# Kernel optimization log

Hardware: AMD Instinct MI355X
Metric: run time of the kernel (lower is better)

The kernel has to match this reference:

```python
import jax, jax.numpy as jnp
import numpy as np

NUM_GRAPHS = 16  # static number of graphs for pooling
BN_EPS = 1e-5


def gat_layer(x, W, a_src, a_dst, src, dst, N, concat):
    # x: (N, Fin), W: (H, Fin, Fout), a_src/a_dst: (H, Fout)
    Wh = jnp.einsum('ni,hio->hno', x, W)                      # (H, N, Fout)
    e_src = jnp.einsum('hno,ho->hn', Wh, a_src)               # (H, N)
    e_dst = jnp.einsum('hno,ho->hn', Wh, a_dst)               # (H, N)
    e = jax.nn.leaky_relu(e_src[:, src] + e_dst[:, dst], 0.2)  # (H, E)
    # edge softmax over incoming edges per dst; torch code starts max at 0
    seg_max = jax.vmap(lambda eh: jax.ops.segment_max(eh, dst, num_segments=N))(e)
    e_max = jnp.maximum(seg_max, 0.0)                         # (H, N)
    exp_e = jnp.exp(e - e_max[:, dst])                        # (H, E)
    exp_sum = jax.vmap(lambda eh: jax.ops.segment_sum(eh, dst, num_segments=N))(exp_e)
    attn = exp_e / (exp_sum[:, dst] + 1e-8)                   # (H, E)
    msgs = attn[:, :, None] * Wh[:, src]                      # (H, E, Fout)
    out = jax.vmap(lambda m: jax.ops.segment_sum(m, dst, num_segments=N))(msgs)  # (H, N, Fout)
    if concat:
        out = jnp.transpose(out, (1, 0, 2)).reshape(N, -1)
    else:
        out = out.mean(axis=0)
    return out, attn


def batchnorm(h, gamma, beta):
    mu = h.mean(axis=0)
    var = h.var(axis=0)
    return (h - mu) / jnp.sqrt(var + BN_EPS) * gamma + beta


def setup_inputs() -> dict:
    key = jax.random.key(0)
    ks = jax.random.split(key, 20)
    N, E = 50000, 400000
    IN, HID, H, NC = 262, 128, 4, 2

    def xavier(k, shape):
        fan_in, fan_out = shape[-2], shape[-1]
        lim = np.sqrt(6.0 / (fan_in + fan_out))
        return jax.random.uniform(k, shape, jnp.float32, -lim, lim)

    x = jax.random.normal(ks[0], (N, IN), jnp.float32)
    edge_index = jax.random.randint(ks[1], (2, E), 0, N, jnp.int64)
    batch = jnp.sort(jax.random.randint(ks[2], (N,), 0, NUM_GRAPHS, jnp.int64))

    return {
        'x': x, 'edge_index': edge_index, 'batch': batch,
        'W1': xavier(ks[3], (H, IN, HID)),
        'a_src1': xavier(ks[4], (H, HID, 1)).squeeze(-1),
        'a_dst1': xavier(ks[5], (H, HID, 1)).squeeze(-1),
        'W2': xavier(ks[6], (1, HID * H, HID)),
        'a_src2': xavier(ks[7], (1, HID, 1)).squeeze(-1),
        'a_dst2': xavier(ks[8], (1, HID, 1)).squeeze(-1),
        'bn1_g': jnp.ones((HID * H,), jnp.float32),
        'bn1_b': jnp.zeros((HID * H,), jnp.float32),
        'bn2_g': jnp.ones((HID,), jnp.float32),
        'bn2_b': jnp.zeros((HID,), jnp.float32),
        'cls_w1': xavier(ks[9], (HID, HID // 2)),
        'cls_b1': jnp.zeros((HID // 2,), jnp.float32),
        'cls_w2': xavier(ks[10], (HID // 2, NC)),
        'cls_b2': jnp.zeros((NC,), jnp.float32),
        'ep_w1': xavier(ks[11], (HID * 2, HID)),
        'ep_b1': jnp.zeros((HID,), jnp.float32),
        'ep_w2': xavier(ks[12], (HID, 1)),
        'ep_b2': jnp.zeros((1,), jnp.float32),
    }


def reference(x, edge_index, batch, W1, a_src1, a_dst1, W2, a_src2, a_dst2,
              bn1_g, bn1_b, bn2_g, bn2_b, cls_w1, cls_b1, cls_w2, cls_b2,
              ep_w1, ep_b1, ep_w2, ep_b2):
    N = x.shape[0]
    src, dst = edge_index[0], edge_index[1]

    h1, _ = gat_layer(x, W1, a_src1, a_dst1, src, dst, N, concat=True)
    h1 = batchnorm(jax.nn.elu(h1), bn1_g, bn1_b)

    h2, attn2 = gat_layer(h1, W2, a_src2, a_dst2, src, dst, N, concat=False)
    h2 = batchnorm(jax.nn.elu(h2), bn2_g, bn2_b)

    # global mean pool over graphs
    sums = jax.ops.segment_sum(h2, batch, num_segments=NUM_GRAPHS)
    counts = jax.ops.segment_sum(jnp.ones((N,), h2.dtype), batch, num_segments=NUM_GRAPHS)
    graph_repr = sums / jnp.clip(counts, 1.0)[:, None]

    logits = jax.nn.relu(graph_repr @ cls_w1 + cls_b1) @ cls_w2 + cls_b2

    edge_feat = jnp.concatenate([h2[src], h2[dst]], axis=1)  # (E, 2*hidden)
    importance = jax.nn.sigmoid(
        (jax.nn.relu(edge_feat @ ep_w1 + ep_b1) @ ep_w2 + ep_b2).squeeze(-1))

    gat_attention = jnp.transpose(attn2, (1, 0))  # (E, 1)
    return logits, h2, importance, gat_attention
```

## Files before the change

### kernel.cpp

```cpp
#include <hip/hip_runtime.h>
#include <hip/hip_bf16.h>
#include <math.h>

typedef __hip_bfloat16 bf16;
typedef __bf16 bf16x8 __attribute__((ext_vector_type(8)));
typedef __bf16 bf16x2v __attribute__((ext_vector_type(2)));
typedef float f32x4 __attribute__((ext_vector_type(4)));

#define NN 50000
#define EE 400000
#define FIN 262
#define KP1 288
#define HID 128
#define NH 4
#define C1 512
#define NGR 16
#define SCAN_NB ((NN + 255) / 256)

__device__ __forceinline__ float b2f(bf16 x){ return __bfloat162float(x); }
__device__ __forceinline__ bf16 f2b(float x){ return __float2bfloat16(x); }
__device__ __forceinline__ float lrelu(float v){ return v >= 0.f ? v : 0.2f * v; }
__device__ __forceinline__ float eluf(float v){ return v > 0.f ? v : expm1f(v); }

__global__ void zero_words(unsigned int* __restrict__ p, int n) {
  int i = blockIdx.x * 256 + threadIdx.x;
  if (i < n) p[i] = 0u;
}

__global__ __launch_bounds__(256)
void gemm_mfma(const bf16* __restrict__ A, const bf16* __restrict__ Bt,
               bf16* __restrict__ C, int M, int K, int Ncols,
               const float* __restrict__ sc, const float* __restrict__ sh) {
  __shared__ __align__(16) __bf16 As[2][128 * 40];
  __shared__ __align__(16) __bf16 Bs[2][128 * 40];
  int bm = blockIdx.y * 128, bn = blockIdx.x * 128;
  int tid = threadIdx.x;
  int wave = tid >> 6, lane = tid & 63;
  int quad = lane >> 4, l16 = lane & 15;
  int wm = (wave >> 1) * 64, wn = (wave & 1) * 64;
  int rowA = (tid * 8) >> 5;
  int colT = (tid * 8) & 31;
  int gm0 = bm + rowA, gm1 = bm + rowA + 64;
  int gn0 = bn + rowA, gn1 = bn + rowA + 64;
  const uint4 zz = {0u, 0u, 0u, 0u};

  f32x4 acc[4][4];
  #pragma unroll
  for (int i = 0; i < 4; ++i)
    #pragma unroll
    for (int j = 0; j < 4; ++j)
      acc[i][j] = (f32x4){0.f, 0.f, 0.f, 0.f};

  uint4 a0, a1, b0, b1;

  auto xf = [&](uint4 v, int kb) -> uint4 {
    if (sc == nullptr) return v;
    bf16x8 a8 = *(bf16x8*)&v;
    float4 c0 = *(const float4*)(sc + kb);
    float4 c1 = *(const float4*)(sc + kb + 4);
    float4 h0 = *(const float4*)(sh + kb);
    float4 h1 = *(const float4*)(sh + kb + 4);
    bf16x8 t8;
    t8[0] = (__bf16)((float)a8[0] * c0.x + h0.x);
    t8[1] = (__bf16)((float)a8[1] * c0.y + h0.y);
    t8[2] = (__bf16)((float)a8[2] * c0.z + h0.z);
    t8[3] = (__bf16)((float)a8[3] * c0.w + h0.w);
    t8[4] = (__bf16)((float)a8[4] * c1.x + h1.x);
    t8[5] = (__bf16)((float)a8[5] * c1.y + h1.y);
    t8[6] = (__bf16)((float)a8[6] * c1.z + h1.z);
    t8[7] = (__bf16)((float)a8[7] * c1.w + h1.w);
    return *(uint4*)&t8;
  };
  auto ld = [&](int k0) {
    a0 = (gm0 < M) ? *(const uint4*)(A + (size_t)gm0 * K + k0 + colT) : zz;
    a1 = (gm1 < M) ? *(const uint4*)(A + (size_t)gm1 * K + k0 + colT) : zz;
    b0 = (gn0 < Ncols) ? *(const uint4*)(Bt + (size_t)gn0 * K + k0 + colT) : zz;
    b1 = (gn1 < Ncols) ? *(const uint4*)(Bt + (size_t)gn1 * K + k0 + colT) : zz;
  };
  auto st = [&](int buf, int k0) {
    *(uint4*)(&As[buf][rowA * 40 + colT])        = xf(a0, k0 + colT);
    *(uint4*)(&As[buf][(rowA + 64) * 40 + colT]) = xf(a1, k0 + colT);
    *(uint4*)(&Bs[buf][rowA * 40 + colT])        = b0;
    *(uint4*)(&Bs[buf][(rowA + 64) * 40 + colT]) = b1;
  };

  int nt = K >> 5;
  ld(0);
  st(0, 0);
  __syncthreads();

  for (int t = 0; t < nt; ++t) {
    int cur = t & 1;
    bool more = (t + 1 < nt);
    if (more) ld((t + 1) << 5);

    bf16x8 af[4], bfr[4];
    #pragma unroll
    for (int i = 0; i < 4; ++i)
      af[i] = *(const bf16x8*)(&As[cur][(wm + i * 16 + l16) * 40 + quad * 8]);
    #pragma unroll
    for (int j = 0; j < 4; ++j)
      bfr[j] = *(const bf16x8*)(&Bs[cur][(wn + j * 16 + l16) * 40 + quad * 8]);
    #pragma unroll
    for (int i = 0; i < 4; ++i)
      #pragma unroll
      for (int j = 0; j < 4; ++j)
        acc[i][j] = __builtin_amdgcn_mfma_f32_16x16x32_bf16(af[i], bfr[j], acc[i][j], 0, 0, 0);

    if (more) st(cur ^ 1, (t + 1) << 5);
    __syncthreads();
  }

  #pragma unroll
  for (int i = 0; i < 4; ++i) {
    #pragma unroll
    for (int r = 0; r < 4; ++r) {
      int gm = bm + wm + i * 16 + quad * 4 + r;
      if (gm >= M) continue;
      #pragma unroll
      for (int j = 0; j < 4; ++j) {
        int gn = bn + wn + j * 16 + l16;
        C[(size_t)gm * Ncols + gn] = f2b(acc[i][j][r]);
      }
    }
  }
}

__global__ void conv_x(const float* __restrict__ x, bf16* __restrict__ xb) {
  int i = blockIdx.x * 256 + threadIdx.x;
  if (i >= NN * KP1) return;
  int row = i / KP1, col = i - row * KP1;
  xb[i] = (col < FIN) ? f2b(x[(size_t)row * FIN + col]) : f2b(0.f);
}
__global__ void prep_b1t(const float* __restrict__ W1, bf16* __restrict__ B1t) {
  int i = blockIdx.x * 256 + threadIdx.x;
  if (i >= C1 * KP1) return;
  int n = i / KP1, k = i - n * KP1;
  int h = n >> 7, o = n & 127;
  B1t[i] = (k < FIN) ? f2b(W1[((size_t)h * FIN + k) * HID + o]) : f2b(0.f);
}
__global__ void prep_b2t(const float* __restrict__ W2, bf16* __restrict__ B2t) {
  int i = blockIdx.x * 256 + threadIdx.x;
  if (i >= HID * C1) return;
  int n = i >> 9, k = i & 511;
  B2t[i] = f2b(W2[(size_t)k * HID + n]);
}
__global__ void prep_bpt(const float* __restrict__ epw1, bf16* __restrict__ BPt) {
  int i = blockIdx.x * 256 + threadIdx.x;
  if (i >= 256 * HID) return;
  int n = i >> 7, k = i & 127;
  float v = (n < 128) ? epw1[(size_t)k * HID + n] : epw1[(size_t)(128 + k) * HID + (n - 128)];
  BPt[i] = f2b(v);
}

__global__ void edot_all(const bf16* __restrict__ Wh1, const float* __restrict__ av,
                         const float* __restrict__ bv, float* __restrict__ es1,
                         float* __restrict__ ed1) {
  int wid = threadIdx.x >> 6, lane = threadIdx.x & 63;
  int n = blockIdx.x * 4 + wid;
  if (n >= NN) return;
  int h = lane >> 4, c16 = lane & 15;
  int fbase = h * HID + c16 * 8;
  bf16x8 r = *(const bf16x8*)(Wh1 + (size_t)n * C1 + fbase);
  float s1 = 0.f, s2 = 0.f;
  #pragma unroll
  for (int j = 0; j < 8; ++j) {
    float rv = (float)r[j];
    s1 += rv * av[fbase + j];
    s2 += rv * bv[fbase + j];
  }
  #pragma unroll
  for (int off = 8; off > 0; off >>= 1) {
    s1 += __shfl_xor(s1, off);
    s2 += __shfl_xor(s2, off);
  }
  if (c16 == 0) { es1[n * 4 + h] = s1; ed1[n * 4 + h] = s2; }
}

__global__ void edot1(const bf16* __restrict__ Wh, const float* __restrict__ av,
                      const float* __restrict__ bv, float* __restrict__ es,
                      float* __restrict__ ed) {
  int wid = threadIdx.x >> 6, lane = threadIdx.x & 63;
  int r = blockIdx.x * 4 + wid;
  if (r >= NN) return;
  const bf16* row = Wh + (size_t)r * HID;
  float w0 = b2f(row[lane]), w1 = b2f(row[lane + 64]);
  float s1 = w0 * av[lane] + w1 * av[lane + 64];
  float s2 = w0 * bv[lane] + w1 * bv[lane + 64];
  #pragma unroll
  for (int off = 32; off > 0; off >>= 1) {
    s1 += __shfl_xor(s1, off);
    s2 += __shfl_xor(s2, off);
  }
  if (lane == 0) { es[r] = s1; ed[r] = s2; }
}

__global__ void count_kernel(const int* __restrict__ dst, int* __restrict__ deg, int E) {
  int e = blockIdx.x * blockDim.x + threadIdx.x;
  if (e >= E) return;
  int d = dst[e];
  if ((unsigned)d < NN) atomicAdd(&deg[d], 1);
}

__global__ void scan_p1(const int* __restrict__ deg, int* __restrict__ bsum) {
  __shared__ int s[256];
  int t = threadIdx.x;
  int i = blockIdx.x * 256 + t;
  s[t] = (i < NN) ? deg[i] : 0;
  __syncthreads();
  #pragma unroll
  for (int off = 128; off > 0; off >>= 1) {
    if (t < off) s[t] += s[t + off];
    __syncthreads();
  }
  if (t == 0) bsum[blockIdx.x] = s[0];
}
__global__ void scan_p2(const int* __restrict__ bsum, int* __restrict__ boff,
                        int* __restrict__ total_out) {
  __shared__ int s[256];
  int t = threadIdx.x;
  s[t] = (t < SCAN_NB) ? bsum[t] : 0;
  __syncthreads();
  if (t == 0) {
    int r = 0;
    for (int i = 0; i < SCAN_NB; ++i) { int v = s[i]; s[i] = r; r += v; }
    total_out[0] = r;
  }
  __syncthreads();
  if (t < SCAN_NB) boff[t] = s[t];
}
__global__ void scan_p3(const int* __restrict__ deg, const int* __restrict__ boff,
                        int* __restrict__ rowptr, int* __restrict__ cursor) {
  __shared__ int s[256];
  int t = threadIdx.x;
  int i = blockIdx.x * 256 + t;
  int v = (i < NN) ? deg[i] : 0;
  s[t] = v;
  __syncthreads();
  #pragma unroll
  for (int off = 1; off < 256; off <<= 1) {
    int add = (t >= off) ? s[t - off] : 0;
    __syncthreads();
    s[t] += add;
    __syncthreads();
  }
  if (i < NN) {
    int pos = boff[blockIdx.x] + s[t] - v;
    rowptr[i] = pos;
    cursor[i] = pos;
  }
}

__global__ void scatter_kernel(const int* __restrict__ src, const int* __restrict__ dst,
                               int* __restrict__ cursor, int* __restrict__ csr_s,
                               int* __restrict__ csr_d, int* __restrict__ csr_e, int E) {
  int e = blockIdx.x * blockDim.x + threadIdx.x;
  if (e >= E) return;
  int d = dst[e];
  if ((unsigned)d >= NN) return;
  int s = src[e]; if ((unsigned)s >= NN) s = 0;
  int p = atomicAdd(&cursor[d], 1);
  if ((unsigned)p < (unsigned)E) { csr_s[p] = s; csr_d[p] = d; csr_e[p] = e; }
}

__global__ void logits1(const int* __restrict__ csr_s, const int* __restrict__ csr_d,
                        const float4* __restrict__ es1, const float4* __restrict__ ed1,
                        float4* __restrict__ v1, int* __restrict__ m1i) {
  int j = blockIdx.x * 256 + threadIdx.x;
  if (j >= EE) return;
  int s = csr_s[j]; if ((unsigned)s >= NN) s = 0;
  int d = csr_d[j]; if ((unsigned)d >= NN) d = 0;
  float4 a = es1[s], bb = ed1[d];
  float4 v;
  v.x = lrelu(a.x + bb.x);
  v.y = lrelu(a.y + bb.y);
  v.z = lrelu(a.z + bb.z);
  v.w = lrelu(a.w + bb.w);
  v1[j] = v;
  if (v.x > 0.f) atomicMax(&m1i[d * 4 + 0], __float_as_int(v.x));
  if (v.y > 0.f) atomicMax(&m1i[d * 4 + 1], __float_as_int(v.y));
  if (v.z > 0.f) atomicMax(&m1i[d * 4 + 2], __float_as_int(v.z));
  if (v.w > 0.f) atomicMax(&m1i[d * 4 + 3], __float_as_int(v.w));
}

__global__ void logits2(const int* __restrict__ csr_s, const int* __restrict__ csr_d,
                        const float* __restrict__ es2, const float* __restrict__ ed2,
                        float* __restrict__ v2, int* __restrict__ m2i) {
  int j = blockIdx.x * 256 + threadIdx.x;
  if (j >= EE) return;
  int s = csr_s[j]; if ((unsigned)s >= NN) s = 0;
  int d = csr_d[j]; if ((unsigned)d >= NN) d = 0;
  float v = lrelu(es2[s] + ed2[d]);
  v2[j] = v;
  if (v > 0.f) atomicMax(&m2i[d], __float_as_int(v));
}

__global__ __launch_bounds__(256, 6)
void agg1_all(const int* __restrict__ csr_s, const int* __restrict__ rowptr,
              const float* __restrict__ lg, const float* __restrict__ mx,
              const bf16* __restrict__ Wh1, bf16* __restrict__ h1) {
  int wid = threadIdx.x >> 6, lane = threadIdx.x & 63;
  int node = blockIdx.x * 4 + wid;
  if (node >= NN) return;
  int b = rowptr[node], e = rowptr[node + 1];
  if (b < 0) b = 0; if (e > EE) e = EE;
  int h = lane >> 4;
  float m = mx[node * 4 + h];
  float sum = 0.f;
  float acc[8] = {};
  const bf16* W = Wh1 + lane * 8;
  int j = b;
  for (; j + 8 <= e; j += 8) {
    int s_[8]; float w[8];
    #pragma unroll
    for (int i = 0; i < 8; ++i) { s_[i] = csr_s[j + i]; w[i] = lg[(j + i) * 4 + h]; }
    bf16x8 r[8];
    #pragma unroll
    for (int i = 0; i < 8; ++i)
      r[i] = *(const bf16x8*)(W + (size_t)s_[i] * C1);
    #pragma unroll
    for (int i = 0; i < 8; ++i) {
      float p = __expf(w[i] - m);
      sum += p;
      #pragma unroll
      for (int k = 0; k < 8; ++k) acc[k] += p * (float)r[i][k];
    }
  }
  if (j + 4 <= e) {
    int s_[4]; float w[4];
    #pragma unroll
    for (int i = 0; i < 4; ++i) { s_[i] = csr_s[j + i]; w[i] = lg[(j + i) * 4 + h]; }
    bf16x8 r[4];
    #pragma unroll
    for (int i = 0; i < 4; ++i)
      r[i] = *(const bf16x8*)(W + (size_t)s_[i] * C1);
    #pragma unroll
    for (int i = 0; i < 4; ++i) {
      float p = __expf(w[i] - m);
      sum += p;
      #pragma unroll
      for (int k = 0; k < 8; ++k) acc[k] += p * (float)r[i][k];
    }
    j += 4;
  }
  for (; j < e; ++j) {
    int s0 = csr_s[j];
    float p = __expf(lg[j * 4 + h] - m);
    bf16x8 r0 = *(const bf16x8*)(W + (size_t)s0 * C1);
    sum += p;
    #pragma unroll
    for (int k = 0; k < 8; ++k) acc[k] += p * (float)r0[k];
  }
  float scale = 1.f / (sum + 1e-8f);
  bf16x8 o;
  #pragma unroll
  for (int k = 0; k < 8; ++k) o[k] = (__bf16)eluf(acc[k] * scale);
  *(bf16x8*)(h1 + (size_t)node * C1 + lane * 8) = o;
}

__global__ __launch_bounds__(256, 8)
void agg2_all(const int* __restrict__ csr_s, const int* __restrict__ rowptr,
              const float* __restrict__ lg, const float* __restrict__ mx,
              const bf16* __restrict__ Wh2, bf16* __restrict__ h2p,
              float* __restrict__ invs2) {
  int tid = threadIdx.x;
  int l16 = tid & 15;
  int node = blockIdx.x * 16 + (tid >> 4);
  if (node >= NN) return;
  int b = rowptr[node], e = rowptr[node + 1];
  if (b < 0) b = 0; if (e > EE) e = EE;
  float m = mx[node];
  float sum = 0.f;
  float acc[8] = {};
  const bf16* W = Wh2 + l16 * 8;
  int j = b;
  for (; j + 4 <= e; j += 4) {
    int s_[4]; float w[4];
    #pragma unroll
    for (int i = 0; i < 4; ++i) { s_[i] = csr_s[j + i]; w[i] = lg[j + i]; }
    bf16x8 r[4];
    #pragma unroll
    for (int i = 0; i < 4; ++i)
      r[i] = *(const bf16x8*)(W + (size_t)s_[i] * HID);
    #pragma unroll
    for (int i = 0; i < 4; ++i) {
      float p = __expf(w[i] - m);
      sum += p;
      #pragma unroll
      for (int k = 0; k < 8; ++k) acc[k] += p * (float)r[i][k];
    }
  }
  for (; j < e; ++j) {
    int s0 = csr_s[j];
    float p = __expf(lg[j] - m);
    bf16x8 r0 = *(const bf16x8*)(W + (size_t)s0 * HID);
    sum += p;
    #pragma unroll
    for (int k = 0; k < 8; ++k) acc[k] += p * (float)r0[k];
  }
  float scale = 1.f / (sum + 1e-8f);
  bf16x8 o;
  #pragma unroll
  for (int k = 0; k < 8; ++k) o[k] = (__bf16)eluf(acc[k] * scale);
  *(bf16x8*)(h2p + (size_t)node * HID + l16 * 8) = o;
  if (l16 == 0) invs2[node] = scale;
}

__global__ void attn_csr(const int* __restrict__ csr_d, const int* __restrict__ csr_e,
                         const float* __restrict__ lg, const float* __restrict__ mx,
                         const float* __restrict__ invs2, float* __restrict__ out) {
  int j = blockIdx.x * 256 + threadIdx.x;
  if (j >= EE) return;
  int d = csr_d[j]; if ((unsigned)d >= NN) d = 0;
  int e = csr_e[j]; if ((unsigned)e >= EE) return;
  out[e] = __expf(lg[j] - mx[d]) * invs2[d];
}

__global__ void stats_ro(const bf16* __restrict__ X, float* __restrict__ cs,
                         float* __restrict__ cq, int Nrows, int C) {
  int c = threadIdx.x;
  int rpb = (Nrows + gridDim.x - 1) / gridDim.x;
  int r0 = blockIdx.x * rpb, r1 = min(r0 + rpb, Nrows);
  float s = 0.f, s2 = 0.f;
  for (int r = r0; r < r1; ++r) {
    float v = b2f(X[(size_t)r * C + c]);
    s += v; s2 += v * v;
  }
  atomicAdd(&cs[c], s);
  atomicAdd(&cq[c], s2);
}

__global__ void bn_coef(const float* __restrict__ cs, const float* __restrict__ cq,
                        const float* __restrict__ gamma, const float* __restrict__ beta,
                        float* __restrict__ sc, float* __restrict__ sh, int C, float invN) {
  int c = blockIdx.x * 256 + threadIdx.x;
  if (c >= C) return;
  float mu = cs[c] * invN;
  float var = cq[c] * invN - mu * mu;
  float g = rsqrtf(fmaxf(var, 0.f) + 1e-5f) * gamma[c];
  sc[c] = g;
  sh[c] = beta[c] - mu * g;
}

__global__ void bn_out(const bf16* __restrict__ in, float* __restrict__ out2,
                       const float* __restrict__ sc, const float* __restrict__ sh) {
  int i = blockIdx.x * 256 + threadIdx.x;
  if (i >= NN * HID / 8) return;
  int c8 = (i & 15) * 8;
  bf16x8 v = *(const bf16x8*)(in + (size_t)i * 8);
  float o[8];
  #pragma unroll
  for (int k = 0; k < 8; ++k) o[k] = (float)v[k] * sc[c8 + k] + sh[c8 + k];
  *(float4*)(out2 + (size_t)i * 8)     = make_float4(o[0], o[1], o[2], o[3]);
  *(float4*)(out2 + (size_t)i * 8 + 4) = make_float4(o[4], o[5], o[6], o[7]);
}

__global__ __launch_bounds__(256)
void pool_kernel(const bf16* __restrict__ h2, const int* __restrict__ batch,
                 float* __restrict__ pooled) {
  int t = threadIdx.x;
  int f = t & 127, half = t >> 7;
  int r0 = blockIdx.x * 32;
  int g_cur = -1;
  float acc = 0.f;
  #pragma unroll
  for (int i = 0; i < 16; ++i) {
    int r = r0 + half + 2 * i;
    if (r >= NN) break;
    int g = batch[r]; if ((unsigned)g >= NGR) g = 0;
    float v = b2f(h2[(size_t)r * HID + f]);
    if (g != g_cur) {
      if (g_cur >= 0) atomicAdd(&pooled[g_cur * HID + f], acc);
      g_cur = g; acc = 0.f;
    }
    acc += v;
  }
  if (g_cur >= 0) atomicAdd(&pooled[g_cur * HID + f], acc);
}

__global__ void cnt_kernel(const int* __restrict__ batch, float* __restrict__ cnt) {
  int g = threadIdx.x;
  if (g >= NGR) return;
  int a = 0, b = NN;
  while (a < b) { int m = (a + b) >> 1; if (batch[m] < g) a = m + 1; else b = m; }
  int lb = a;
  a = 0; b = NN;
  while (a < b) { int m = (a + b) >> 1; if (batch[m] <= g) a = m + 1; else b = m; }
  cnt[g] = (float)(a - lb);
}

__global__ void cls_kernel(const float* __restrict__ pooled, const float* __restrict__ cnt,
                           const float* __restrict__ sc2, const float* __restrict__ sh2,
                           const float* __restrict__ w1, const float* __restrict__ b1,
                           const float* __restrict__ w2, const float* __restrict__ b2,
                           float* __restrict__ out) {
  __shared__ float repr[NGR * HID];
  __shared__ float hid[NGR * 64];
  int t = threadIdx.x;
  for (int i = t; i < NGR * HID; i += 128) {
    int g = i >> 7, c = i & 127;
    float c_ = cnt[g];
    repr[i] = (c_ > 0.f) ? (pooled[i] / c_ * sc2[c] + sh2[c]) : 0.f;
  }
  __syncthreads();
  for (int i = t; i < NGR * 64; i += 128) {
    int g = i >> 6, j = i & 63;
    float s = b1[j];
    for (int c = 0; c < HID; ++c) s += repr[g * HID + c] * w1[c * 64 + j];
    hid[i] = fmaxf(s, 0.f);
  }
  __syncthreads();
  if (t < NGR * 2) {
    int g = t >> 1, k = t & 1;
    float s = b2[k];
    for (int j = 0; j < 64; ++j) s += hid[g * 64 + j] * w2[j * 2 + k];
    out[t] = s;
  }
}

__global__ __launch_bounds__(256)
void eimp_kernel(const int* __restrict__ csr_s, const int* __restrict__ csr_d,
                 const int* __restrict__ csr_e, const bf16* __restrict__ PQ,
                 const float* __restrict__ b1, const float* __restrict__ w2,
                 const float* __restrict__ b2, float* __restrict__ out) {
  int tid = threadIdx.x;
  int wave = tid >> 6, lane = tid & 63;
  int g = lane >> 4, l16 = lane & 15;
  int slot = blockIdx.x * 16 + wave * 4 + g;
  if (slot >= EE) return;
  int s = csr_s[slot]; if ((unsigned)s >= NN) s = 0;
  int d = csr_d[slot]; if ((unsigned)d >= NN) d = 0;
  int e = csr_e[slot]; if ((unsigned)e >= EE) return;
  bf16x8 p = *(const bf16x8*)(PQ + (size_t)s * 256 + l16 * 8);
  bf16x8 q = *(const bf16x8*)(PQ + (size_t)d * 256 + 128 + l16 * 8);
  float acc = 0.f;
  #pragma unroll
  for (int r = 0; r < 8; ++r) {
    int jj = l16 * 8 + r;
    float hh = (float)p[r] + (float)q[r] + b1[jj];
    hh = fmaxf(hh, 0.f);
    acc += hh * w2[jj];
  }
  #pragma unroll
  for (int off = 8; off > 0; off >>= 1) acc += __shfl_xor(acc, off);
  if (l16 == 0) {
    float z = acc + b2[0];
    out[e] = 1.f / (1.f + expf(-z));
  }
}

extern "C" void kernel_launch(void* const* d_in, const int* in_sizes, int n_in,
                              void* d_out, int out_size, void* d_ws, size_t ws_size,
                              hipStream_t stream) {
  const float* x      = (const float*)d_in[0];
  const int*   ei     = (const int*)d_in[1];
  const int*   batch  = (const int*)d_in[2];
  const float* W1     = (const float*)d_in[3];
  const float* a_src1 = (const float*)d_in[4];
  const float* a_dst1 = (const float*)d_in[5];
  const float* W2     = (const float*)d_in[6];
  const float* a_src2 = (const float*)d_in[7];
  const float* a_dst2 = (const float*)d_in[8];
  const float* bn1_g  = (const float*)d_in[9];
  const float* bn1_b  = (const float*)d_in[10];
  const float* bn2_g  = (const float*)d_in[11];
  const float* bn2_b  = (const float*)d_in[12];
  const float* cls_w1 = (const float*)d_in[13];
  const float* cls_b1 = (const float*)d_in[14];
  const float* cls_w2 = (const float*)d_in[15];
  const float* cls_b2 = (const float*)d_in[16];
  const float* ep_w1  = (const float*)d_in[17];
  const float* ep_b1  = (const float*)d_in[18];
  const float* ep_w2  = (const float*)d_in[19];
  const float* ep_b2  = (const float*)d_in[20];

  const int* srcp = ei;
  const int* dstp = ei + EE;

  char* base = (char*)d_ws;
  bf16* xb   = (bf16*)(base);
  bf16* h1   = (bf16*)(base);
  bf16* Wh1  = (bf16*)(base + 51200000);
  bf16* Wh2  = (bf16*)(base + 51200000);
  bf16* PQ   = (bf16*)(base + 51200000);
  bf16* h2p  = (bf16*)(base + 76800000);
  float* es1   = (float*)(base + 102400000);
  float* ed1   = (float*)(base + 103200000);
  float* v2csr = (float*)(base + 102400000);
  int*   m1i   = (int*)(base + 104000000);
  int*   m2i   = (int*)(base + 104800000);
  int*   deg   = (int*)(base + 105000000);
  float* stats = (float*)(base + 105200000);
  float* cs1 = stats,        *cq1 = stats + 512;
  float* cs2 = stats + 1024, *cq2 = stats + 1152;
  float* pooled = stats + 1280;
  float* cnt    = stats + 3328;
  float* sc1   = (float*)(base + 105213376);
  float* sh1   = (float*)(base + 105215424);
  float* sc2   = (float*)(base + 105217472);
  float* sh2   = (float*)(base + 105217984);
  float* es2   = (float*)(base + 105218496);
  float* ed2   = (float*)(base + 105418496);
  float* invs2 = (float*)(base + 105618496);
  int*   cursor= (int*)(base + 105818496);
  int*   rowptr= (int*)(base + 106018496);
  int*   bsum  = (int*)(base + 106218560);
  int*   boff  = bsum + 256;
  int*   csr_s = (int*)(base + 106220608);
  int*   csr_d = (int*)(base + 107820608);
  int*   csr_e = (int*)(base + 109420608);
  float* v1csr = (float*)(base + 111020608);
  bf16*  B1t   = (bf16*)(base + 117420608);
  bf16*  B2t   = (bf16*)(base + 117715520);
  bf16*  BPt   = (bf16*)(base + 117846592);

  float* out        = (float*)d_out;
  float* out_logits = out;
  float* out_h2     = out + 32;
  float* out_imp    = out + 32 + (size_t)NN * HID;
  float* out_attn   = out_imp + EE;

  zero_words<<<(303344 + 255) / 256, 256, 0, stream>>>((unsigned int*)m1i, 303344);

  conv_x<<<(NN * KP1 + 255) / 256, 256, 0, stream>>>(x, xb);
  prep_b1t<<<(C1 * KP1 + 255) / 256, 256, 0, stream>>>(W1, B1t);
  prep_b2t<<<(HID * C1 + 255) / 256, 256, 0, stream>>>(W2, B2t);
  prep_bpt<<<(256 * HID + 255) / 256, 256, 0, stream>>>(ep_w1, BPt);

  count_kernel<<<(EE + 255) / 256, 256, 0, stream>>>(dstp, deg, EE);
  scan_p1<<<SCAN_NB, 256, 0, stream>>>(deg, bsum);
  scan_p2<<<1, 256, 0, stream>>>(bsum, boff, rowptr + NN);
  scan_p3<<<SCAN_NB, 256, 0, stream>>>(deg, boff, rowptr, cursor);
  scatter_kernel<<<(EE + 255) / 256, 256, 0, stream>>>(srcp, dstp, cursor,
                                                       csr_s, csr_d, csr_e, EE);

  dim3 g1(C1 / 128, (NN + 127) / 128);
  gemm_mfma<<<g1, 256, 0, stream>>>(xb, B1t, Wh1, NN, KP1, C1, nullptr, nullptr);
  edot_all<<<(NN + 3) / 4, 256, 0, stream>>>(Wh1, a_src1, a_dst1, es1, ed1);
  logits1<<<(EE + 255) / 256, 256, 0, stream>>>(csr_s, csr_d, (const float4*)es1,
                                                (const float4*)ed1, (float4*)v1csr, m1i);
  agg1_all<<<(NN + 3) / 4, 256, 0, stream>>>(csr_s, rowptr, v1csr,
                                             (const float*)m1i, Wh1, h1);

  stats_ro<<<400, C1, 0, stream>>>(h1, cs1, cq1, NN, C1);
  bn_coef<<<2, 256, 0, stream>>>(cs1, cq1, bn1_g, bn1_b, sc1, sh1, C1, 1.f / NN);

  dim3 g2(1, (NN + 127) / 128);
  gemm_mfma<<<g2, 256, 0, stream>>>(h1, B2t, Wh2, NN, C1, HID, sc1, sh1);
  edot1<<<(NN + 3) / 4, 256, 0, stream>>>(Wh2, a_src2, a_dst2, es2, ed2);
  logits2<<<(EE + 255) / 256, 256, 0, stream>>>(csr_s, csr_d, es2, ed2, v2csr, m2i);
  agg2_all<<<(NN + 15) / 16, 256, 0, stream>>>(csr_s, rowptr, v2csr,
                                               (const float*)m2i, Wh2, h2p, invs2);
  attn_csr<<<(EE + 255) / 256, 256, 0, stream>>>(csr_d, csr_e, v2csr,
                                                 (const float*)m2i, invs2, out_attn);

  pool_kernel<<<(NN + 31) / 32, 256, 0, stream>>>(h2p, batch, pooled);
  cnt_kernel<<<1, 64, 0, stream>>>(batch, cnt);

  stats_ro<<<400, HID, 0, stream>>>(h2p, cs2, cq2, NN, HID);
  bn_coef<<<1, 256, 0, stream>>>(cs2, cq2, bn2_g, bn2_b, sc2, sh2, HID, 1.f / NN);
  bn_out<<<(NN * HID / 8 + 255) / 256, 256, 0, stream>>>(h2p, out_h2, sc2, sh2);

  cls_kernel<<<1, 128, 0, stream>>>(pooled, cnt, sc2, sh2,
                                    cls_w1, cls_b1, cls_w2, cls_b2, out_logits);

  dim3 gpq(2, (NN + 127) / 128);
  gemm_mfma<<<gpq, 256, 0, stream>>>(h2p, BPt, PQ, NN, HID, 256, sc2, sh2);
  eimp_kernel<<<(EE + 15) / 16, 256, 0, stream>>>(csr_s, csr_d, csr_e, PQ,
                                                  ep_b1, ep_w2, ep_b2, out_imp);
}
```

Measured before the change: 654.3 us.

## Fuse fp32 conversion and attention dots into GEMM, merge pool with BN output

The first GEMM now reads fp32 x directly and converts it to bf16 while staging into shared memory, which removes the separate conv_x pass and its bf16 buffer. Both GAT GEMMs compute the per-node attention dot products (e_src, e_dst) in their epilogue, reducing across lanes and accumulating with atomics, so the edot kernels go away. The BN2 output write is folded into the pooling kernel, and the count kernel is merged into the classifier kernel. In exchange, the fp32 A loads use narrower float2 accesses with bounds checks, and the atomic accumulation requires zeroing a larger region.

Result: no change. 644.7 us (-1.5%).

```diff
diff --git a/kernel.cpp b/kernel.cpp
--- a/kernel.cpp
+++ b/kernel.cpp
@@ -28,9 +28,12 @@
 }
 
 __global__ __launch_bounds__(256)
-void gemm_mfma(const bf16* __restrict__ A, const bf16* __restrict__ Bt,
-               bf16* __restrict__ C, int M, int K, int Ncols,
-               const float* __restrict__ sc, const float* __restrict__ sh) {
+void gemm_mfma(const bf16* __restrict__ A, const float* __restrict__ Af32, int srcW,
+               const bf16* __restrict__ Bt, bf16* __restrict__ C,
+               int M, int K, int Ncols,
+               const float* __restrict__ sc, const float* __restrict__ sh,
+               const float* __restrict__ av, const float* __restrict__ bv,
+               float* __restrict__ esp, float* __restrict__ edp, int dstride) {
   __shared__ __align__(16) __bf16 As[2][128 * 40];
   __shared__ __align__(16) __bf16 Bs[2][128 * 40];
   int bm = blockIdx.y * 128, bn = blockIdx.x * 128;
@@ -52,6 +55,7 @@
       acc[i][j] = (f32x4){0.f, 0.f, 0.f, 0.f};
 
   uint4 a0, a1, b0, b1;
+  float fa0[8], fa1[8];
 
   auto xf = [&](uint4 v, int kb) -> uint4 {
     if (sc == nullptr) return v;
@@ -71,15 +75,38 @@
     t8[7] = (__bf16)((float)a8[7] * c1.w + h1.w);
     return *(uint4*)&t8;
   };
+  auto ldf = [&](float* F, int gm, int k0) {
+    #pragma unroll
+    for (int p = 0; p < 4; ++p) {
+      int col = k0 + colT + p * 2;
+      float2 v = make_float2(0.f, 0.f);
+      if (gm < M && col < srcW)
+        v = *(const float2*)(Af32 + (size_t)gm * srcW + col);
+      F[p * 2] = v.x; F[p * 2 + 1] = v.y;
+    }
+  };
   auto ld = [&](int k0) {
-    a0 = (gm0 < M) ? *(const uint4*)(A + (size_t)gm0 * K + k0 + colT) : zz;
-    a1 = (gm1 < M) ? *(const uint4*)(A + (size_t)gm1 * K + k0 + colT) : zz;
+    if (Af32) {
+      ldf(fa0, gm0, k0);
+      ldf(fa1, gm1, k0);
+    } else {
+      a0 = (gm0 < M) ? *(const uint4*)(A + (size_t)gm0 * K + k0 + colT) : zz;
+      a1 = (gm1 < M) ? *(const uint4*)(A + (size_t)gm1 * K + k0 + colT) : zz;
+    }
     b0 = (gn0 < Ncols) ? *(const uint4*)(Bt + (size_t)gn0 * K + k0 + colT) : zz;
     b1 = (gn1 < Ncols) ? *(const uint4*)(Bt + (size_t)gn1 * K + k0 + colT) : zz;
   };
   auto st = [&](int buf, int k0) {
-    *(uint4*)(&As[buf][rowA * 40 + colT])        = xf(a0, k0 + colT);
-    *(uint4*)(&As[buf][(rowA + 64) * 40 + colT]) = xf(a1, k0 + colT);
+    if (Af32) {
+      bf16x8 t0, t1;
+      #pragma unroll
+      for (int p = 0; p < 8; ++p) { t0[p] = (__bf16)fa0[p]; t1[p] = (__bf16)fa1[p]; }
+      *(uint4*)(&As[buf][rowA * 40 + colT])        = *(uint4*)&t0;
+      *(uint4*)(&As[buf][(rowA + 64) * 40 + colT]) = *(uint4*)&t1;
+    } else {
+      *(uint4*)(&As[buf][rowA * 40 + colT])        = xf(a0, k0 + colT);
+      *(uint4*)(&As[buf][(rowA + 64) * 40 + colT]) = xf(a1, k0 + colT);
+    }
     *(uint4*)(&Bs[buf][rowA * 40 + colT])        = b0;
     *(uint4*)(&Bs[buf][(rowA + 64) * 40 + colT]) = b1;
   };
@@ -124,14 +151,39 @@
       }
     }
   }
-}
-
-__global__ void conv_x(const float* __restrict__ x, bf16* __restrict__ xb) {
-  int i = blockIdx.x * 256 + threadIdx.x;
-  if (i >= NN * KP1) return;
-  int row = i / KP1, col = i - row * KP1;
-  xb[i] = (col < FIN) ? f2b(x[(size_t)row * FIN + col]) : f2b(0.f);
-}
+
+  if (esp) {
+    float avj[4], bvj[4];
+    #pragma unroll
+    for (int j = 0; j < 4; ++j) {
+      int gn = bn + wn + j * 16 + l16;
+      avj[j] = av[gn]; bvj[j] = bv[gn];
+    }
+    int hoff = (dstride == 4) ? (bn >> 7) : 0;
+    #pragma unroll
+    for (int i = 0; i < 4; ++i)
+      #pragma unroll
+      for (int r = 0; r < 4; ++r) {
+        float pa = 0.f, pb = 0.f;
+        #pragma unroll
+        for (int j = 0; j < 4; ++j) {
+          float v = acc[i][j][r];
+          pa += v * avj[j]; pb += v * bvj[j];
+        }
+        #pragma unroll
+        for (int off = 8; off > 0; off >>= 1) {
+          pa += __shfl_xor(pa, off);
+          pb += __shfl_xor(pb, off);
+        }
+        int gm = bm + wm + i * 16 + quad * 4 + r;
+        if (l16 == 0 && gm < M) {
+          atomicAdd(&esp[gm * dstride + hoff], pa);
+          atomicAdd(&edp[gm * dstride + hoff], pb);
+        }
+      }
+  }
+}
+
 __global__ void prep_b1t(const float* __restrict__ W1, bf16* __restrict__ B1t) {
   int i = blockIdx.x * 256 + threadIdx.x;
   if (i >= C1 * KP1) return;
@@ -151,48 +203,6 @@
   int n = i >> 7, k = i & 127;
   float v = (n < 128) ? epw1[(size_t)k * HID + n] : epw1[(size_t)(128 + k) * HID + (n - 128)];
   BPt[i] = f2b(v);
-}
-
-__global__ void edot_all(const bf16* __restrict__ Wh1, const float* __restrict__ av,
-                         const float* __restrict__ bv, float* __restrict__ es1,
-                         float* __restrict__ ed1) {
-  int wid = threadIdx.x >> 6, lane = threadIdx.x & 63;
-  int n = blockIdx.x * 4 + wid;
-  if (n >= NN) return;
-  int h = lane >> 4, c16 = lane & 15;
-  int fbase = h * HID + c16 * 8;
-  bf16x8 r = *(const bf16x8*)(Wh1 + (size_t)n * C1 + fbase);
-  float s1 = 0.f, s2 = 0.f;
-  #pragma unroll
-  for (int j = 0; j < 8; ++j) {
-    float rv = (float)r[j];
-    s1 += rv * av[fbase + j];
-    s2 += rv * bv[fbase + j];
-  }
-  #pragma unroll
-  for (int off = 8; off > 0; off >>= 1) {
-    s1 += __shfl_xor(s1, off);
-    s2 += __shfl_xor(s2, off);
-  }
-  if (c16 == 0) { es1[n * 4 + h] = s1; ed1[n * 4 + h] = s2; }
-}
-
-__global__ void edot1(const bf16* __restrict__ Wh, const float* __restrict__ av,
-                      const float* __restrict__ bv, float* __restrict__ es,
-                      float* __restrict__ ed) {
-  int wid = threadIdx.x >> 6, lane = threadIdx.x & 63;
-  int r = blockIdx.x * 4 + wid;
-  if (r >= NN) return;
-  const bf16* row = Wh + (size_t)r * HID;
-  float w0 = b2f(row[lane]), w1 = b2f(row[lane + 64]);
-  float s1 = w0 * av[lane] + w1 * av[lane + 64];
-  float s2 = w0 * bv[lane] + w1 * bv[lane + 64];
-  #pragma unroll
-  for (int off = 32; off > 0; off >>= 1) {
-    s1 += __shfl_xor(s1, off);
-    s2 += __shfl_xor(s2, off);
-  }
-  if (lane == 0) { es[r] = s1; ed[r] = s2; }
 }
 
 __global__ void count_kernel(const int* __restrict__ dst, int* __restrict__ deg, int E) {
@@ -442,24 +452,13 @@
   sh[c] = beta[c] - mu * g;
 }
 
-__global__ void bn_out(const bf16* __restrict__ in, float* __restrict__ out2,
-                       const float* __restrict__ sc, const float* __restrict__ sh) {
-  int i = blockIdx.x * 256 + threadIdx.x;
-  if (i >= NN * HID / 8) return;
-  int c8 = (i & 15) * 8;
-  bf16x8 v = *(const bf16x8*)(in + (size_t)i * 8);
-  float o[8];
-  #pragma unroll
-  for (int k = 0; k < 8; ++k) o[k] = (float)v[k] * sc[c8 + k] + sh[c8 + k];
-  *(float4*)(out2 + (size_t)i * 8)     = make_float4(o[0], o[1], o[2], o[3]);
-  *(float4*)(out2 + (size_t)i * 8 + 4) = make_float4(o[4], o[5], o[6], o[7]);
-}
-
 __global__ __launch_bounds__(256)
-void pool_kernel(const bf16* __restrict__ h2, const int* __restrict__ batch,
-                 float* __restrict__ pooled) {
+void poolbn_kernel(const bf16* __restrict__ h2p, const int* __restrict__ batch,
+                   const float* __restrict__ sc, const float* __restrict__ sh,
+                   float* __restrict__ out_h2, float* __restrict__ pooled) {
   int t = threadIdx.x;
   int f = t & 127, half = t >> 7;
+  float scf = sc[f], shf = sh[f];
   int r0 = blockIdx.x * 32;
   int g_cur = -1;
   float acc = 0.f;
@@ -468,7 +467,8 @@
     int r = r0 + half + 2 * i;
     if (r >= NN) break;
     int g = batch[r]; if ((unsigned)g >= NGR) g = 0;
-    float v = b2f(h2[(size_t)r * HID + f]);
+    float v = b2f(h2p[(size_t)r * HID + f]) * scf + shf;
+    out_h2[(size_t)r * HID + f] = v;
     if (g != g_cur) {
       if (g_cur >= 0) atomicAdd(&pooled[g_cur * HID + f], acc);
       g_cur = g; acc = 0.f;
@@ -478,29 +478,27 @@
   if (g_cur >= 0) atomicAdd(&pooled[g_cur * HID + f], acc);
 }
 
-__global__ void cnt_kernel(const int* __restrict__ batch, float* __restrict__ cnt) {
-  int g = threadIdx.x;
-  if (g >= NGR) return;
-  int a = 0, b = NN;
-  while (a < b) { int m = (a + b) >> 1; if (batch[m] < g) a = m + 1; else b = m; }
-  int lb = a;
-  a = 0; b = NN;
-  while (a < b) { int m = (a + b) >> 1; if (batch[m] <= g) a = m + 1; else b = m; }
-  cnt[g] = (float)(a - lb);
-}
-
-__global__ void cls_kernel(const float* __restrict__ pooled, const float* __restrict__ cnt,
-                           const float* __restrict__ sc2, const float* __restrict__ sh2,
+__global__ void cls_kernel(const float* __restrict__ pooled, const int* __restrict__ batch,
                            const float* __restrict__ w1, const float* __restrict__ b1,
                            const float* __restrict__ w2, const float* __restrict__ b2,
                            float* __restrict__ out) {
   __shared__ float repr[NGR * HID];
   __shared__ float hid[NGR * 64];
+  __shared__ float scnt[NGR];
   int t = threadIdx.x;
+  if (t < NGR) {
+    int g = t;
+    int a = 0, b = NN;
+    while (a < b) { int m = (a + b) >> 1; if (batch[m] < g) a = m + 1; else b = m; }
+    int lb = a;
+    a = 0; b = NN;
+    while (a < b) { int m = (a + b) >> 1; if (batch[m] <= g) a = m + 1; else b = m; }
+    scnt[t] = (float)(a - lb);
+  }
+  __syncthreads();
   for (int i = t; i < NGR * HID; i += 128) {
-    int g = i >> 7, c = i & 127;
-    float c_ = cnt[g];
-    repr[i] = (c_ > 0.f) ? (pooled[i] / c_ * sc2[c] + sh2[c]) : 0.f;
+    int g = i >> 7;
+    repr[i] = pooled[i] / fmaxf(scnt[g], 1.f);
   }
   __syncthreads();
   for (int i = t; i < NGR * 64; i += 128) {
@@ -578,7 +576,6 @@
   const int* dstp = ei + EE;
 
   char* base = (char*)d_ws;
-  bf16* xb   = (bf16*)(base);
   bf16* h1   = (bf16*)(base);
   bf16* Wh1  = (bf16*)(base + 51200000);
   bf16* Wh2  = (bf16*)(base + 51200000);
@@ -587,20 +584,19 @@
   float* es1   = (float*)(base + 102400000);
   float* ed1   = (float*)(base + 103200000);
   float* v2csr = (float*)(base + 102400000);
-  int*   m1i   = (int*)(base + 104000000);
-  int*   m2i   = (int*)(base + 104800000);
-  int*   deg   = (int*)(base + 105000000);
-  float* stats = (float*)(base + 105200000);
+  float* es2   = (float*)(base + 104000000);
+  float* ed2   = (float*)(base + 104200000);
+  int*   m1i   = (int*)(base + 104400000);
+  int*   m2i   = (int*)(base + 105200000);
+  int*   deg   = (int*)(base + 105400000);
+  float* stats = (float*)(base + 105600000);
   float* cs1 = stats,        *cq1 = stats + 512;
   float* cs2 = stats + 1024, *cq2 = stats + 1152;
   float* pooled = stats + 1280;
-  float* cnt    = stats + 3328;
-  float* sc1   = (float*)(base + 105213376);
-  float* sh1   = (float*)(base + 105215424);
-  float* sc2   = (float*)(base + 105217472);
-  float* sh2   = (float*)(base + 105217984);
-  float* es2   = (float*)(base + 105218496);
-  float* ed2   = (float*)(base + 105418496);
+  float* sc1   = (float*)(base + 105613376);
+  float* sh1   = (float*)(base + 105615424);
+  float* sc2   = (float*)(base + 105617472);
+  float* sh2   = (float*)(base + 105617984);
   float* invs2 = (float*)(base + 105618496);
   int*   cursor= (int*)(base + 105818496);
   int*   rowptr= (int*)(base + 106018496);
@@ -620,9 +616,8 @@
   float* out_imp    = out + 32 + (size_t)NN * HID;
   float* out_attn   = out_imp + EE;
 
-  zero_words<<<(303344 + 255) / 256, 256, 0, stream>>>((unsigned int*)m1i, 303344);
-
-  conv_x<<<(NN * KP1 + 255) / 256, 256, 0, stream>>>(x, xb);
+  zero_words<<<(803344 + 255) / 256, 256, 0, stream>>>((unsigned int*)es1, 803344);
+
   prep_b1t<<<(C1 * KP1 + 255) / 256, 256, 0, stream>>>(W1, B1t);
   prep_b2t<<<(HID * C1 + 255) / 256, 256, 0, stream>>>(W2, B2t);
   prep_bpt<<<(256 * HID + 255) / 256, 256, 0, stream>>>(ep_w1, BPt);
@@ -635,8 +630,8 @@
                                                        csr_s, csr_d, csr_e, EE);
 
   dim3 g1(C1 / 128, (NN + 127) / 128);
-  gemm_mfma<<<g1, 256, 0, stream>>>(xb, B1t, Wh1, NN, KP1, C1, nullptr, nullptr);
-  edot_all<<<(NN + 3) / 4, 256, 0, stream>>>(Wh1, a_src1, a_dst1, es1, ed1);
+  gemm_mfma<<<g1, 256, 0, stream>>>(nullptr, x, FIN, B1t, Wh1, NN, KP1, C1,
+                                    nullptr, nullptr, a_src1, a_dst1, es1, ed1, 4);
   logits1<<<(EE + 255) / 256, 256, 0, stream>>>(csr_s, csr_d, (const float4*)es1,
                                                 (const float4*)ed1, (float4*)v1csr, m1i);
   agg1_all<<<(NN + 3) / 4, 256, 0, stream>>>(csr_s, rowptr, v1csr,
@@ -646,26 +641,24 @@
   bn_coef<<<2, 256, 0, stream>>>(cs1, cq1, bn1_g, bn1_b, sc1, sh1, C1, 1.f / NN);
 
   dim3 g2(1, (NN + 127) / 128);
-  gemm_mfma<<<g2, 256, 0, stream>>>(h1, B2t, Wh2, NN, C1, HID, sc1, sh1);
-  edot1<<<(NN + 3) / 4, 256, 0, stream>>>(Wh2, a_src2, a_dst2, es2, ed2);
+  gemm_mfma<<<g2, 256, 0, stream>>>(h1, nullptr, 0, B2t, Wh2, NN, C1, HID,
+                                    sc1, sh1, a_src2, a_dst2, es2, ed2, 1);
   logits2<<<(EE + 255) / 256, 256, 0, stream>>>(csr_s, csr_d, es2, ed2, v2csr, m2i);
   agg2_all<<<(NN + 15) / 16, 256, 0, stream>>>(csr_s, rowptr, v2csr,
                                                (const float*)m2i, Wh2, h2p, invs2);
   attn_csr<<<(EE + 255) / 256, 256, 0, stream>>>(csr_d, csr_e, v2csr,
                                                  (const float*)m2i, invs2, out_attn);
 
-  pool_kernel<<<(NN + 31) / 32, 256, 0, stream>>>(h2p, batch, pooled);
-  cnt_kernel<<<1, 64, 0, stream>>>(batch, cnt);
-
   stats_ro<<<400, HID, 0, stream>>>(h2p, cs2, cq2, NN, HID);
   bn_coef<<<1, 256, 0, stream>>>(cs2, cq2, bn2_g, bn2_b, sc2, sh2, HID, 1.f / NN);
-  bn_out<<<(NN * HID / 8 + 255) / 256, 256, 0, stream>>>(h2p, out_h2, sc2, sh2);
-
-  cls_kernel<<<1, 128, 0, stream>>>(pooled, cnt, sc2, sh2,
-                                    cls_w1, cls_b1, cls_w2, cls_b2, out_logits);
+
+  poolbn_kernel<<<(NN + 31) / 32, 256, 0, stream>>>(h2p, batch, sc2, sh2, out_h2, pooled);
+  cls_kernel<<<1, 128, 0, stream>>>(pooled, batch, cls_w1, cls_b1, cls_w2, cls_b2,
+                                    out_logits);
 
   dim3 gpq(2, (NN + 127) / 128);
-  gemm_mfma<<<gpq, 256, 0, stream>>>(h2p, BPt, PQ, NN, HID, 256, sc2, sh2);
+  gemm_mfma<<<gpq, 256, 0, stream>>>(h2p, nullptr, 0, BPt, PQ, NN, HID, 256,
+                                     sc2, sh2, nullptr, nullptr, nullptr, nullptr, 0);
   eimp_kernel<<<(EE + 15) / 16, 256, 0, stream>>>(csr_s, csr_d, csr_e, PQ,
                                                   ep_b1, ep_w2, ep_b2, out_imp);
 }
```
